# Performance work log

Measured on AMD Instinct MI355X. Metric: run time of the kernel, lower is better.

The kernel has to match this reference:

```python
import jax, jax.numpy as jnp
import numpy as np

B, A, M, NCLS = 8, 100000, 100, 80
EPS = 1e-4


def setup_inputs() -> dict:
    key = jax.random.key(0)
    k1, k2, k3, k4, k5, k6, k7 = jax.random.split(key, 7)
    # predictions: [B, 4+1+classes, A]
    dt = jax.random.normal(k1, (B, 5 + NCLS, A), dtype=jnp.float32)
    # gt: [B, M, 5] = (x1, y1, w, h, class in 1..NCLS); padded entries are still
    # valid positive boxes so logs are finite (they are masked out of the loss).
    xy = jax.random.uniform(k2, (B, M, 2), minval=0.0, maxval=600.0)
    wh = jax.random.uniform(k3, (B, M, 2), minval=4.0, maxval=128.0)
    cls = jax.random.randint(k4, (B, M, 1), 1, NCLS + 1).astype(jnp.float32)
    gt = jnp.concatenate([xy, wh, cls], axis=-1)
    # anchors: [A, 4] in xyxy with positive width/height
    axy = jax.random.uniform(k5, (A, 2), minval=0.0, maxval=600.0)
    awh = jax.random.uniform(k6, (A, 2), minval=8.0, maxval=128.0)
    anchors = jnp.concatenate([axy, axy + awh], axis=-1)
    # assignment: -1 ignore, 0 background, k>=1 -> gt box index k-1
    assign_result = jax.random.randint(k7, (B, A), -1, M + 1).astype(jnp.int32)
    return {"dt": dt, "gt": gt, "anchors": anchors, "assign_result": assign_result}


def reference(dt, gt, anchors, assign_result):
    classes = dt.shape[1] - 5
    batch_size = dt.shape[0]
    af = assign_result.astype(jnp.float32)                  # [B, A]

    anch_w = anchors[:, 2] - anchors[:, 0]                  # [A]
    anch_h = anchors[:, 3] - anchors[:, 1]
    anch_x = anchors[:, 0] + 0.5 * anch_w
    anch_y = anchors[:, 1] + 0.5 * anch_h

    pos_cls = af >= -0.1                                    # assigned or background
    pos_box = af >= 0.9                                     # assigned to a gt box
    n_cls = pos_cls.sum(-1).astype(jnp.float32)             # [B]
    n_box = pos_box.sum(-1).astype(jnp.float32)

    # gather assigned gt annotation per anchor (clipped index; masked later)
    idx = jnp.clip(assign_result - 1, 0, gt.shape[1] - 1)   # [B, A]
    assigned = jnp.take_along_axis(gt, idx[..., None], axis=1)  # [B, A, 5]

    # ---- classification (BCE-style on objectness + one-hot class targets) ----
    obj_t = jnp.clip(af, 0.0, 1.0)                          # [B, A]
    oh = jax.nn.one_hot(assigned[..., 4].astype(jnp.int32) - 1, classes,
                        dtype=jnp.float32)                  # [B, A, C]
    oh = jnp.where(pos_box[..., None], oh, 0.0)
    tgt = jnp.concatenate([obj_t[..., None], oh], axis=-1)  # [B, A, 1+C]
    tgt = jnp.clip(tgt, EPS, 1.0 - EPS)
    dt_cls = jnp.clip(jnp.swapaxes(dt[:, 4:, :], 1, 2), EPS, 1.0 - EPS)  # [B, A, 1+C]
    cls_per = (-dt_cls * jnp.log(tgt) + (dt_cls - 1.0) * jnp.log(1.0 - tgt)).sum(-1)
    cls_loss = jnp.where(pos_cls, cls_per, 0.0).sum(-1) / jnp.maximum(n_cls, 1.0)

    ann_w = assigned[..., 2]
    ann_h = assigned[..., 3]
    ann_x = assigned[..., 0] + 0.5 * ann_w
    ann_y = assigned[..., 1] + 0.5 * ann_h
    tx = (ann_x - anch_x) / anch_w                          # [B, A]
    ty = (ann_y - anch_y) / anch_h
    tw = jnp.log(ann_w / anch_w)
    th = jnp.log(ann_h / anch_h)
    targets = jnp.stack([tx, ty, tw, th], axis=1)           # [B, 4, A]
    box_per = jnp.square(targets - dt[:, 0:4, :])           # [B, 4, A]
    box_sum = jnp.where(pos_box[:, None, :], box_per, 0.0).sum((1, 2))
    box_loss = jnp.where(n_box > 0, box_sum / jnp.maximum(n_box, 1.0), 0.0)

    return (box_loss.sum() + cls_loss.sum()) / batch_size
```

## Files before the change

### kernel.cpp

```cpp
#include <hip/hip_runtime.h>
#include <math.h>

constexpr int kB  = 8;
constexpr int kA  = 100000;
constexpr int kM  = 100;
constexpr int kCH = 85;
constexpr float kEPS = 1e-4f;

#define L0 (-9.210340371976182f)
#define L1 (-1.0000500033334732e-4f)

__device__ __forceinline__ float wave_reduce_f(float v) {
#pragma unroll
    for (int off = 32; off > 0; off >>= 1) v += __shfl_down(v, off, 64);
    return v;
}
__device__ __forceinline__ int wave_reduce_i(int v) {
#pragma unroll
    for (int off = 32; off > 0; off >>= 1) v += __shfl_down(v, off, 64);
    return v;
}

__global__ __launch_bounds__(256) void loss_main(
    const float* __restrict__ dt, const float* __restrict__ gt,
    const float* __restrict__ anchors, const int* __restrict__ assign,
    float* __restrict__ ws_f, int* __restrict__ ws_i)
{
    const int b = blockIdx.y;
    const int a = blockIdx.x * blockDim.x + threadIdx.x;

    float cls_c = 0.f, box_c = 0.f;
    int ncls_c = 0, nbox_c = 0;

    if (a < kA) {
        const int as = assign[b * kA + a];
        if (as >= 0) {
            const float* dp = dt + (size_t)b * kCH * kA + a;
            float P = 0.f;
#pragma unroll 9
            for (int c = 4; c < kCH; ++c) {
                float x = dp[(size_t)c * kA];
                x = fminf(fmaxf(x, kEPS), 1.0f - kEPS);
                P += x;
            }
            float per = (L1 - L0) * P - 81.0f * L1;
            if (as >= 1) {
                const int idx = min(as - 1, kM - 1);
                const float* g = gt + ((size_t)b * kM + idx) * 5;
                const float g0 = g[0], g1 = g[1], g2 = g[2], g3 = g[3];
                const int cls = (int)g[4];
                float p_obj = fminf(fmaxf(dp[(size_t)4 * kA], kEPS), 1.0f - kEPS);
                float p_cls = fminf(fmaxf(dp[(size_t)(4 + cls) * kA], kEPS), 1.0f - kEPS);
                per += (2.0f * (p_obj + p_cls) - 2.0f) * (L0 - L1);

                const float4 av = ((const float4*)anchors)[a];
                const float aw = av.z - av.x, ah = av.w - av.y;
                const float ax = av.x + 0.5f * aw, ay = av.y + 0.5f * ah;
                const float gx = g0 + 0.5f * g2, gy = g1 + 0.5f * g3;
                const float d0 = (gx - ax) / aw - dp[0];
                const float d1 = (gy - ay) / ah - dp[(size_t)1 * kA];
                const float d2 = logf(g2 / aw) - dp[(size_t)2 * kA];
                const float d3 = logf(g3 / ah) - dp[(size_t)3 * kA];
                box_c = d0 * d0 + d1 * d1 + d2 * d2 + d3 * d3;
                nbox_c = 1;
            }
            cls_c = per;
            ncls_c = 1;
        }
    }

    __shared__ float s_cls[4], s_box[4];
    __shared__ int   s_nc[4], s_nb[4];
    cls_c  = wave_reduce_f(cls_c);
    box_c  = wave_reduce_f(box_c);
    ncls_c = wave_reduce_i(ncls_c);
    nbox_c = wave_reduce_i(nbox_c);
    const int lane = threadIdx.x & 63, wid = threadIdx.x >> 6;
    if (lane == 0) { s_cls[wid] = cls_c; s_box[wid] = box_c; s_nc[wid] = ncls_c; s_nb[wid] = nbox_c; }
    __syncthreads();
    if (threadIdx.x == 0) {
        float cs = 0.f, bs = 0.f; int nc = 0, nb = 0;
#pragma unroll
        for (int w = 0; w < 4; ++w) { cs += s_cls[w]; bs += s_box[w]; nc += s_nc[w]; nb += s_nb[w]; }
        atomicAdd(&ws_f[b * 2 + 0], cs);
        atomicAdd(&ws_f[b * 2 + 1], bs);
        atomicAdd(&ws_i[b * 2 + 0], nc);
        atomicAdd(&ws_i[b * 2 + 1], nb);
    }
}

__global__ void loss_final(const float* __restrict__ ws_f,
                           const int* __restrict__ ws_i,
                           float* __restrict__ out)
{
    if (threadIdx.x == 0 && blockIdx.x == 0) {
        float tot = 0.f;
#pragma unroll
        for (int b = 0; b < kB; ++b) {
            const float cls_sum = ws_f[b * 2 + 0];
            const float box_sum = ws_f[b * 2 + 1];
            const float n_cls = (float)ws_i[b * 2 + 0];
            const float n_box = (float)ws_i[b * 2 + 1];
            const float cls_loss = cls_sum / fmaxf(n_cls, 1.0f);
            const float box_loss = (n_box > 0.f) ? box_sum / fmaxf(n_box, 1.0f) : 0.f;
            tot += cls_loss + box_loss;
        }
        out[0] = tot / (float)kB;
    }
}

extern "C" void kernel_launch(void* const* d_in, const int* in_sizes, int n_in,
                              void* d_out, int out_size, void* d_ws, size_t ws_size,
                              hipStream_t stream) {
    const float* dt      = (const float*)d_in[0];
    const float* gt      = (const float*)d_in[1];
    const float* anchors = (const float*)d_in[2];
    const int*   assign  = (const int*)d_in[3];
    float* out = (float*)d_out;

    float* ws_f = (float*)d_ws;
    int*   ws_i = (int*)(ws_f + 2 * kB);

    hipMemsetAsync(d_ws, 0, (2 * kB) * sizeof(float) + (2 * kB) * sizeof(int), stream);

    dim3 grid((kA + 255) / 256, kB);
    loss_main<<<grid, 256, 0, stream>>>(dt, gt, anchors, assign, ws_f, ws_i);
    loss_final<<<1, 64, 0, stream>>>(ws_f, ws_i, out);
}
```

Measured before the change: 403.3 us.

## Vectorize anchor processing to float4 and replace atomics with per-block partials

Each thread now handles four consecutive anchors, reading every channel row with float4 loads. The channel data is read unconditionally rather than skipped for ignored anchors. Per-block sums are written to a partials array and reduced by a 512-thread final kernel, which removes the global atomics and the memset. The wider loads aim to cut load instruction count and improve bandwidth use, at the cost of reading dt for ignored anchors (about 1%) and higher register pressure.

```diff
diff --git a/kernel.cpp b/kernel.cpp
--- a/kernel.cpp
+++ b/kernel.cpp
@@ -7,15 +7,17 @@
 constexpr int kCH = 85;
 constexpr float kEPS = 1e-4f;
 
+constexpr int kA4 = kA / 4;
+constexpr int kGX = (kA4 + 255) / 256;
+
 #define L0 (-9.210340371976182f)
 #define L1 (-1.0000500033334732e-4f)
 
+__device__ __forceinline__ float clipf(float x) {
+    return fminf(fmaxf(x, kEPS), 1.0f - kEPS);
+}
+
 __device__ __forceinline__ float wave_reduce_f(float v) {
-#pragma unroll
-    for (int off = 32; off > 0; off >>= 1) v += __shfl_down(v, off, 64);
-    return v;
-}
-__device__ __forceinline__ int wave_reduce_i(int v) {
 #pragma unroll
     for (int off = 32; off > 0; off >>= 1) v += __shfl_down(v, off, 64);
     return v;
@@ -24,87 +26,118 @@
 __global__ __launch_bounds__(256) void loss_main(
     const float* __restrict__ dt, const float* __restrict__ gt,
     const float* __restrict__ anchors, const int* __restrict__ assign,
-    float* __restrict__ ws_f, int* __restrict__ ws_i)
+    float4* __restrict__ partials)
 {
     const int b = blockIdx.y;
-    const int a = blockIdx.x * blockDim.x + threadIdx.x;
+    const int i = blockIdx.x * 256 + threadIdx.x;
 
-    float cls_c = 0.f, box_c = 0.f;
-    int ncls_c = 0, nbox_c = 0;
+    float cls_c = 0.f, box_c = 0.f, ncls_c = 0.f, nbox_c = 0.f;
 
-    if (a < kA) {
-        const int as = assign[b * kA + a];
-        if (as >= 0) {
-            const float* dp = dt + (size_t)b * kCH * kA + a;
-            float P = 0.f;
-#pragma unroll 9
-            for (int c = 4; c < kCH; ++c) {
-                float x = dp[(size_t)c * kA];
-                x = fminf(fmaxf(x, kEPS), 1.0f - kEPS);
-                P += x;
-            }
-            float per = (L1 - L0) * P - 81.0f * L1;
-            if (as >= 1) {
-                const int idx = min(as - 1, kM - 1);
+    if (i < kA4) {
+        const int4 as4 = ((const int4*)(assign + (size_t)b * kA))[i];
+        const int as[4] = {as4.x, as4.y, as4.z, as4.w};
+
+        const float4* dp4 = (const float4*)(dt + (size_t)b * kCH * kA) + i;
+
+        const float4 d0 = dp4[0];
+        const float4 d1 = dp4[(size_t)1 * kA4];
+        const float4 d2 = dp4[(size_t)2 * kA4];
+        const float4 d3 = dp4[(size_t)3 * kA4];
+
+        const float4 v4 = dp4[(size_t)4 * kA4];
+        const float pobj[4] = {clipf(v4.x), clipf(v4.y), clipf(v4.z), clipf(v4.w)};
+        float P[4] = {pobj[0], pobj[1], pobj[2], pobj[3]};
+
+#pragma unroll 10
+        for (int c = 5; c < kCH; ++c) {
+            const float4 u = dp4[(size_t)c * kA4];
+            P[0] += clipf(u.x);
+            P[1] += clipf(u.y);
+            P[2] += clipf(u.z);
+            P[3] += clipf(u.w);
+        }
+
+        const float d0a[4] = {d0.x, d0.y, d0.z, d0.w};
+        const float d1a[4] = {d1.x, d1.y, d1.z, d1.w};
+        const float d2a[4] = {d2.x, d2.y, d2.z, d2.w};
+        const float d3a[4] = {d3.x, d3.y, d3.z, d3.w};
+
+#pragma unroll
+        for (int j = 0; j < 4; ++j) {
+            const int as_j = as[j];
+            if (as_j < 0) continue;
+            float per = (L1 - L0) * P[j] - 81.0f * L1;
+            if (as_j >= 1) {
+                const int idx = min(as_j - 1, kM - 1);
                 const float* g = gt + ((size_t)b * kM + idx) * 5;
                 const float g0 = g[0], g1 = g[1], g2 = g[2], g3 = g[3];
                 const int cls = (int)g[4];
-                float p_obj = fminf(fmaxf(dp[(size_t)4 * kA], kEPS), 1.0f - kEPS);
-                float p_cls = fminf(fmaxf(dp[(size_t)(4 + cls) * kA], kEPS), 1.0f - kEPS);
-                per += (2.0f * (p_obj + p_cls) - 2.0f) * (L0 - L1);
 
-                const float4 av = ((const float4*)anchors)[a];
+                const float p_cls =
+                    clipf(dt[((size_t)b * kCH + 4 + cls) * kA + 4 * i + j]);
+                per += (2.0f * (pobj[j] + p_cls) - 2.0f) * (L0 - L1);
+
+                const float4 av = ((const float4*)anchors)[4 * i + j];
                 const float aw = av.z - av.x, ah = av.w - av.y;
                 const float ax = av.x + 0.5f * aw, ay = av.y + 0.5f * ah;
-                const float gx = g0 + 0.5f * g2, gy = g1 + 0.5f * g3;
-                const float d0 = (gx - ax) / aw - dp[0];
-                const float d1 = (gy - ay) / ah - dp[(size_t)1 * kA];
-                const float d2 = logf(g2 / aw) - dp[(size_t)2 * kA];
-                const float d3 = logf(g3 / ah) - dp[(size_t)3 * kA];
-                box_c = d0 * d0 + d1 * d1 + d2 * d2 + d3 * d3;
-                nbox_c = 1;
+                const float t0 = (g0 + 0.5f * g2 - ax) / aw - d0a[j];
+                const float t1 = (g1 + 0.5f * g3 - ay) / ah - d1a[j];
+                const float t2 = logf(g2 / aw) - d2a[j];
+                const float t3 = logf(g3 / ah) - d3a[j];
+                box_c += t0 * t0 + t1 * t1 + t2 * t2 + t3 * t3;
+                nbox_c += 1.f;
             }
-            cls_c = per;
-            ncls_c = 1;
+            cls_c += per;
+            ncls_c += 1.f;
         }
     }
 
-    __shared__ float s_cls[4], s_box[4];
-    __shared__ int   s_nc[4], s_nb[4];
     cls_c  = wave_reduce_f(cls_c);
     box_c  = wave_reduce_f(box_c);
-    ncls_c = wave_reduce_i(ncls_c);
-    nbox_c = wave_reduce_i(nbox_c);
+    ncls_c = wave_reduce_f(ncls_c);
+    nbox_c = wave_reduce_f(nbox_c);
+
+    __shared__ float4 s[4];
     const int lane = threadIdx.x & 63, wid = threadIdx.x >> 6;
-    if (lane == 0) { s_cls[wid] = cls_c; s_box[wid] = box_c; s_nc[wid] = ncls_c; s_nb[wid] = nbox_c; }
+    if (lane == 0) s[wid] = make_float4(cls_c, box_c, ncls_c, nbox_c);
     __syncthreads();
     if (threadIdx.x == 0) {
-        float cs = 0.f, bs = 0.f; int nc = 0, nb = 0;
+        float4 t = s[0];
 #pragma unroll
-        for (int w = 0; w < 4; ++w) { cs += s_cls[w]; bs += s_box[w]; nc += s_nc[w]; nb += s_nb[w]; }
-        atomicAdd(&ws_f[b * 2 + 0], cs);
-        atomicAdd(&ws_f[b * 2 + 1], bs);
-        atomicAdd(&ws_i[b * 2 + 0], nc);
-        atomicAdd(&ws_i[b * 2 + 1], nb);
+        for (int w = 1; w < 4; ++w) {
+            t.x += s[w].x; t.y += s[w].y; t.z += s[w].z; t.w += s[w].w;
+        }
+        partials[(size_t)b * kGX + blockIdx.x] = t;
     }
 }
 
-__global__ void loss_final(const float* __restrict__ ws_f,
-                           const int* __restrict__ ws_i,
-                           float* __restrict__ out)
+__global__ __launch_bounds__(512) void loss_final(
+    const float4* __restrict__ partials, float* __restrict__ out)
 {
-    if (threadIdx.x == 0 && blockIdx.x == 0) {
+    const int wid  = threadIdx.x >> 6;
+    const int lane = threadIdx.x & 63;
+
+    float cls = 0.f, box = 0.f, nc = 0.f, nb = 0.f;
+    for (int e = lane; e < kGX; e += 64) {
+        const float4 p = partials[(size_t)wid * kGX + e];
+        cls += p.x; box += p.y; nc += p.z; nb += p.w;
+    }
+    cls = wave_reduce_f(cls);
+    box = wave_reduce_f(box);
+    nc  = wave_reduce_f(nc);
+    nb  = wave_reduce_f(nb);
+
+    __shared__ float s_loss[8];
+    if (lane == 0) {
+        const float cl = cls / fmaxf(nc, 1.0f);
+        const float bl = (nb > 0.f) ? box / fmaxf(nb, 1.0f) : 0.f;
+        s_loss[wid] = cl + bl;
+    }
+    __syncthreads();
+    if (threadIdx.x == 0) {
         float tot = 0.f;
 #pragma unroll
-        for (int b = 0; b < kB; ++b) {
-            const float cls_sum = ws_f[b * 2 + 0];
-            const float box_sum = ws_f[b * 2 + 1];
-            const float n_cls = (float)ws_i[b * 2 + 0];
-            const float n_box = (float)ws_i[b * 2 + 1];
-            const float cls_loss = cls_sum / fmaxf(n_cls, 1.0f);
-            const float box_loss = (n_box > 0.f) ? box_sum / fmaxf(n_box, 1.0f) : 0.f;
-            tot += cls_loss + box_loss;
-        }
+        for (int bb = 0; bb < kB; ++bb) tot += s_loss[bb];
         out[0] = tot / (float)kB;
     }
 }
@@ -118,12 +151,9 @@
     const int*   assign  = (const int*)d_in[3];
     float* out = (float*)d_out;
 
-    float* ws_f = (float*)d_ws;
-    int*   ws_i = (int*)(ws_f + 2 * kB);
+    float4* partials = (float4*)d_ws;
 
-    hipMemsetAsync(d_ws, 0, (2 * kB) * sizeof(float) + (2 * kB) * sizeof(int), stream);
-
-    dim3 grid((kA + 255) / 256, kB);
-    loss_main<<<grid, 256, 0, stream>>>(dt, gt, anchors, assign, ws_f, ws_i);
-    loss_final<<<1, 64, 0, stream>>>(ws_f, ws_i, out);
+    dim3 grid(kGX, kB);
+    loss_main<<<grid, 256, 0, stream>>>(dt, gt, anchors, assign, partials);
+    loss_final<<<1, 512, 0, stream>>>(partials, out);
 }
```

New measurement: 384.0 us (median of 2 runs). 4.8% less time.
